# Kernel optimization log

Hardware: AMD Instinct MI355X
Metric: run time of the kernel (lower is better)

## Reference

```python
import jax, jax.numpy as jnp
import numpy as np

B, T, D_IN, H, NL = 4096, 512, 32, 16, 2


def setup_inputs() -> dict:
    key = jax.random.key(0)
    ks = jax.random.split(key, 16)
    s = lambda fan: 1.0 / np.sqrt(H)  # PyTorch LSTM init scale: U(-1/sqrt(H), 1/sqrt(H))
    u = lambda k, shape: jax.random.uniform(k, shape, jnp.float32, -s(H), s(H))
    inp = {
        "x": jax.random.normal(ks[0], (B, T, D_IN), jnp.float32),
        # layer 0 (gate order i, f, g, o as in PyTorch)
        "Wih0": u(ks[1], (4 * H, D_IN)),
        "Whh0": u(ks[2], (4 * H, H)),
        "bih0": u(ks[3], (4 * H,)),
        "bhh0": u(ks[4], (4 * H,)),
        # layer 1
        "Wih1": u(ks[5], (4 * H, H)),
        "Whh1": u(ks[6], (4 * H, H)),
        "bih1": u(ks[7], (4 * H,)),
        "bhh1": u(ks[8], (4 * H,)),
        # MLP head
        "fc1_w": u(ks[9], (8, H)),
        "fc1_b": u(ks[10], (8,)),
        "fc2_w": u(ks[11], (1, 8)),
        "fc2_b": u(ks[12], (1,)),
    }
    return inp


def _lstm_layer(x_seq, Wih, Whh, bih, bhh):
    # x_seq: [B, T, D]; returns all hidden states [B, T, H]
    b = bih + bhh
    # precompute input projections for all timesteps: [T, B, 4H]
    xg = jnp.einsum("btd,gd->tbg", x_seq, Wih) + b
    h0 = jnp.zeros((x_seq.shape[0], H), x_seq.dtype)
    c0 = jnp.zeros_like(h0)

    def step(carry, xt):
        h, c = carry
        gates = xt + h @ Whh.T  # [B, 4H]
        i, f, g, o = jnp.split(gates, 4, axis=-1)
        i, f, o = jax.nn.sigmoid(i), jax.nn.sigmoid(f), jax.nn.sigmoid(o)
        g = jnp.tanh(g)
        c = f * c + i * g
        h = o * jnp.tanh(c)
        return (h, c), h

    _, hs = jax.lax.scan(step, (h0, c0), xg)  # hs: [T, B, H]
    return jnp.transpose(hs, (1, 0, 2))


def reference(x, Wih0, Whh0, bih0, bhh0, Wih1, Whh1, bih1, bhh1, fc1_w, fc1_b, fc2_w, fc2_b):
    h1 = _lstm_layer(x, Wih0, Whh0, bih0, bhh0)   # [B, T, H]
    h2 = _lstm_layer(h1, Wih1, Whh1, bih1, bhh1)  # [B, T, H]
    last = h2[:, -1, :]                            # [B, H]
    y = jax.nn.relu(last @ fc1_w.T + fc1_b)        # [B, 8]
    return y @ fc2_w.T + fc2_b                     # [B, 1]
```

## Files before the change

kernel.cpp:

```cpp
#include <hip/hip_runtime.h>
#include <stdint.h>

#define T_STEPS 512
#define D_INP   32
#define CHUNK   8
#define NCHUNK  (T_STEPS / CHUNK)

typedef float f2 __attribute__((ext_vector_type(2)));
typedef float f4 __attribute__((ext_vector_type(4)));

typedef const uint32_t __attribute__((address_space(1)))* gas1_t;
typedef uint32_t __attribute__((address_space(3)))* las3_t;

#define LOG2E 1.44269504088896f
#define TANHK (-2.88539008177793f)

template <int K>
__device__ __forceinline__ float qbcast(float v) {
  return __int_as_float(
      __builtin_amdgcn_mov_dpp(__float_as_int(v), K * 85, 0xF, 0xF, true));
}

__device__ __forceinline__ float frcp(float v) { return __builtin_amdgcn_rcpf(v); }
__device__ __forceinline__ float fexp2(float v) { return __builtin_amdgcn_exp2f(v); }
__device__ __forceinline__ f2 lo2(f4 v) { return __builtin_shufflevector(v, v, 0, 1); }
__device__ __forceinline__ f2 hi2(f4 v) { return __builtin_shufflevector(v, v, 2, 3); }
__device__ __forceinline__ f2 pkfma(f2 a, f2 b, f2 c) {
  return __builtin_elementwise_fma(a, b, c);
}

extern "C" __global__ void __launch_bounds__(256)
lstm2_fused(const float* __restrict__ x,
            const float* __restrict__ Wih0, const float* __restrict__ Whh0,
            const float* __restrict__ bih0, const float* __restrict__ bhh0,
            const float* __restrict__ Wih1, const float* __restrict__ Whh1,
            const float* __restrict__ bih1, const float* __restrict__ bhh1,
            const float* __restrict__ fc1w, const float* __restrict__ fc1b,
            const float* __restrict__ fc2w, const float* __restrict__ fc2b,
            float* __restrict__ out)
{
  __shared__ __align__(16) float lx[4][2][CHUNK * D_INP];
  __shared__ __align__(16) float lh0[4][80];
  __shared__ __align__(16) float lh1[4][80];

  const int tid  = threadIdx.x;
  const int w    = tid >> 6;
  const int lane = tid & 63;
  const int b    = (blockIdx.x << 2) + w;

  const int k   = lane & 3;
  const int u   = lane >> 2;
  const int row = k * 16 + u;

  const float sc = (k == 2) ? -2.0f * LOG2E : -LOG2E;
  const float mA = (k == 2) ?  2.0f : 1.0f;
  const float aA = (k == 2) ? -1.0f : 0.0f;

  f2 wi0[16], wh0[8], wi1[8], wh1[8];
  {
    const f4* p = (const f4*)(Wih0 + row * 32);
#pragma unroll
    for (int q = 0; q < 8; ++q) {
      f4 v = p[q];
      wi0[2 * q + 0] = lo2(v) * sc;
      wi0[2 * q + 1] = hi2(v) * sc;
    }
    const f4* p0 = (const f4*)(Whh0 + row * 16);
    const f4* p1 = (const f4*)(Wih1 + row * 16);
    const f4* p2 = (const f4*)(Whh1 + row * 16);
#pragma unroll
    for (int q = 0; q < 4; ++q) {
      f4 a = p0[q], bq = p1[q], cq = p2[q];
      wh0[2 * q] = lo2(a) * sc;  wh0[2 * q + 1] = hi2(a) * sc;
      wi1[2 * q] = lo2(bq) * sc; wi1[2 * q + 1] = hi2(bq) * sc;
      wh1[2 * q] = lo2(cq) * sc; wh1[2 * q + 1] = hi2(cq) * sc;
    }
  }
  const float bs0 = sc * (bih0[row] + bhh0[row]);
  const float bs1 = sc * (bih1[row] + bhh1[row]);

  const int slot = (k == 0) ? u : (16 + lane);
  float* h0slot = &lh0[w][slot];
  float* h1slot = &lh1[w][slot];

  float c0 = 0.f, c1 = 0.f;
  f2 h0p[8];
#pragma unroll
  for (int j = 0; j < 8; ++j) h0p[j] = (f2){0.f, 0.f};
  if (lane < 16) lh1[w][lane] = 0.f;

  const float* xg = x + (size_t)b * (T_STEPS * D_INP);

  {
    const float* src = xg + lane * 4;
    __builtin_amdgcn_global_load_lds((gas1_t)(const void*)src,
                                     (las3_t)(void*)&lx[w][0][0], 16, 0, 0);
  }

#pragma unroll 1
  for (int c = 0; c < NCHUNK; ++c) {
    asm volatile("s_waitcnt vmcnt(0)" ::: "memory");
    if (c + 1 < NCHUNK) {
      const float* src = xg + (c + 1) * (CHUNK * D_INP) + lane * 4;
      __builtin_amdgcn_global_load_lds((gas1_t)(const void*)src,
                                       (las3_t)(void*)&lx[w][(c + 1) & 1][0],
                                       16, 0, 0);
    }
    const float* xp = &lx[w][c & 1][0];
#pragma unroll
    for (int tt = 0; tt < CHUNK; ++tt) {
      const float* xq = xp + tt * D_INP;
      f4 hA = *(const f4*)(&lh1[w][0]);
      f4 hB = *(const f4*)(&lh1[w][4]);
      f4 hC = *(const f4*)(&lh1[w][8]);
      f4 hD = *(const f4*)(&lh1[w][12]);
      f2 b01 = (f2){bs1, 0.f}, b23 = (f2){0.f, 0.f};
      b01 = pkfma(wh1[0], lo2(hA), b01);  b23 = pkfma(wh1[1], hi2(hA), b23);
      b01 = pkfma(wh1[2], lo2(hB), b01);  b23 = pkfma(wh1[3], hi2(hB), b23);
      b01 = pkfma(wh1[4], lo2(hC), b01);  b23 = pkfma(wh1[5], hi2(hC), b23);
      b01 = pkfma(wh1[6], lo2(hD), b01);  b23 = pkfma(wh1[7], hi2(hD), b23);
      f2 a01 = (f2){bs0, 0.f}, a23 = (f2){0.f, 0.f};
#pragma unroll
      for (int q = 0; q < 8; ++q) {
        f4 v = *(const f4*)(xq + 4 * q);
        a01 = pkfma(wi0[2 * q + 0], lo2(v), a01);
        a23 = pkfma(wi0[2 * q + 1], hi2(v), a23);
      }
#pragma unroll
      for (int q = 0; q < 4; ++q) {
        a01 = pkfma(wh0[2 * q + 0], h0p[2 * q + 0], a01);
        a23 = pkfma(wh0[2 * q + 1], h0p[2 * q + 1], a23);
      }
      f2 asum = a01 + a23;
      float gs = asum.x + asum.y;
      float av = fmaf(mA, frcp(1.f + fexp2(gs)), aA);
      float fv = qbcast<1>(av), gv = qbcast<2>(av), ov = qbcast<3>(av);
      c0 = fmaf(fv, c0, av * gv);
      float th = fmaf(2.f, frcp(1.f + fexp2(TANHK * c0)), -1.f);
      float h0n = ov * th;
      *h0slot = h0n;
#pragma unroll
      for (int q = 0; q < 4; ++q) {
        f4 hv = *(const f4*)(&lh0[w][4 * q]);
        h0p[2 * q + 0] = lo2(hv);
        h0p[2 * q + 1] = hi2(hv);
      }
#pragma unroll
      for (int q = 0; q < 4; ++q) {
        b01 = pkfma(wi1[2 * q + 0], h0p[2 * q + 0], b01);
        b23 = pkfma(wi1[2 * q + 1], h0p[2 * q + 1], b23);
      }
      f2 bsum = b01 + b23;
      float gs1 = bsum.x + bsum.y;
      float av1 = fmaf(mA, frcp(1.f + fexp2(gs1)), aA);
      float fv1 = qbcast<1>(av1), gv1 = qbcast<2>(av1), ov1 = qbcast<3>(av1);
      c1 = fmaf(fv1, c1, av1 * gv1);
      float th1 = fmaf(2.f, frcp(1.f + fexp2(TANHK * c1)), -1.f);
      float h1n = ov1 * th1;
      *h1slot = h1n;
    }
  }

  float h1f[16];
#pragma unroll
  for (int q = 0; q < 4; ++q) {
    f4 hv = *(const f4*)(&lh1[w][4 * q]);
#pragma unroll
    for (int r = 0; r < 4; ++r) h1f[4 * q + r] = hv[r];
  }
  float rr = 0.f;
  if (lane < 8) {
    float acc = fc1b[lane];
#pragma unroll
    for (int j = 0; j < 16; ++j) acc = fmaf(fc1w[lane * 16 + j], h1f[j], acc);
    rr = fmaxf(acc, 0.f) * fc2w[lane];
  }
  rr += __shfl_xor(rr, 1, 64);
  rr += __shfl_xor(rr, 2, 64);
  rr += __shfl_xor(rr, 4, 64);
  if (lane == 0) out[b] = rr + fc2b[0];
}

extern "C" void kernel_launch(void* const* d_in, const int* in_sizes, int n_in,
                              void* d_out, int out_size, void* d_ws, size_t ws_size,
                              hipStream_t stream) {
  (void)in_sizes; (void)n_in; (void)d_ws; (void)ws_size; (void)out_size;
  const float* x    = (const float*)d_in[0];
  const float* Wih0 = (const float*)d_in[1];
  const float* Whh0 = (const float*)d_in[2];
  const float* bih0 = (const float*)d_in[3];
  const float* bhh0 = (const float*)d_in[4];
  const float* Wih1 = (const float*)d_in[5];
  const float* Whh1 = (const float*)d_in[6];
  const float* bih1 = (const float*)d_in[7];
  const float* bhh1 = (const float*)d_in[8];
  const float* fc1w = (const float*)d_in[9];
  const float* fc1b = (const float*)d_in[10];
  const float* fc2w = (const float*)d_in[11];
  const float* fc2b = (const float*)d_in[12];
  lstm2_fused<<<dim3(1024), dim3(256), 0, stream>>>(
      x, Wih0, Whh0, bih0, bhh0, Wih1, Whh1, bih1, bhh1,
      fc1w, fc1b, fc2w, fc2b, (float*)d_out);
}
```

Baseline: 408.7 us.

## Split LSTM layers across two wavefronts with chunked LDS ring pipeline

Each block now handles one batch element with two wavefronts. Wave 0 runs layer 0 and writes each chunk of hidden states into a double-buffered LDS ring, while wave 1 runs layer 1 on the previous chunk, and the two sync once per chunk. This shortens the per-step serial dependency chain of each wave and lets the two layers overlap. The cost is twice as many waves per batch element, a block-wide barrier every chunk, and one chunk of extra pipeline latency.

```diff
diff --git a/kernel.cpp b/kernel.cpp
--- a/kernel.cpp
+++ b/kernel.cpp
@@ -29,24 +29,25 @@
   return __builtin_elementwise_fma(a, b, c);
 }
 
-extern "C" __global__ void __launch_bounds__(256)
-lstm2_fused(const float* __restrict__ x,
-            const float* __restrict__ Wih0, const float* __restrict__ Whh0,
-            const float* __restrict__ bih0, const float* __restrict__ bhh0,
-            const float* __restrict__ Wih1, const float* __restrict__ Whh1,
-            const float* __restrict__ bih1, const float* __restrict__ bhh1,
-            const float* __restrict__ fc1w, const float* __restrict__ fc1b,
-            const float* __restrict__ fc2w, const float* __restrict__ fc2b,
-            float* __restrict__ out)
+extern "C" __global__ void __launch_bounds__(128)
+lstm2_pipe(const float* __restrict__ x,
+           const float* __restrict__ Wih0, const float* __restrict__ Whh0,
+           const float* __restrict__ bih0, const float* __restrict__ bhh0,
+           const float* __restrict__ Wih1, const float* __restrict__ Whh1,
+           const float* __restrict__ bih1, const float* __restrict__ bhh1,
+           const float* __restrict__ fc1w, const float* __restrict__ fc1b,
+           const float* __restrict__ fc2w, const float* __restrict__ fc2b,
+           float* __restrict__ out)
 {
-  __shared__ __align__(16) float lx[4][2][CHUNK * D_INP];
-  __shared__ __align__(16) float lh0[4][80];
-  __shared__ __align__(16) float lh1[4][80];
+  __shared__ __align__(16) float lx[2][CHUNK * D_INP];
+  __shared__ __align__(16) float ring[2][CHUNK][16];
+  __shared__ __align__(16) float dump[64];
+  __shared__ __align__(16) float lh1[80];
 
   const int tid  = threadIdx.x;
   const int w    = tid >> 6;
   const int lane = tid & 63;
-  const int b    = (blockIdx.x << 2) + w;
+  const int b    = blockIdx.x;
 
   const int k   = lane & 3;
   const int u   = lane >> 2;
@@ -56,129 +57,165 @@
   const float mA = (k == 2) ?  2.0f : 1.0f;
   const float aA = (k == 2) ? -1.0f : 0.0f;
 
-  f2 wi0[16], wh0[8], wi1[8], wh1[8];
-  {
-    const f4* p = (const f4*)(Wih0 + row * 32);
-#pragma unroll
-    for (int q = 0; q < 8; ++q) {
-      f4 v = p[q];
-      wi0[2 * q + 0] = lo2(v) * sc;
-      wi0[2 * q + 1] = hi2(v) * sc;
-    }
-    const f4* p0 = (const f4*)(Whh0 + row * 16);
-    const f4* p1 = (const f4*)(Wih1 + row * 16);
-    const f4* p2 = (const f4*)(Whh1 + row * 16);
+  if (w == 0) {
+    f2 wi0[16], wh0[8];
+    {
+      const f4* p = (const f4*)(Wih0 + row * 32);
+#pragma unroll
+      for (int q = 0; q < 8; ++q) {
+        f4 v = p[q];
+        wi0[2 * q + 0] = lo2(v) * sc;
+        wi0[2 * q + 1] = hi2(v) * sc;
+      }
+      const f4* p0 = (const f4*)(Whh0 + row * 16);
+#pragma unroll
+      for (int q = 0; q < 4; ++q) {
+        f4 a = p0[q];
+        wh0[2 * q] = lo2(a) * sc;  wh0[2 * q + 1] = hi2(a) * sc;
+      }
+    }
+    const float bs0 = sc * (bih0[row] + bhh0[row]);
+    float c0 = 0.f;
+    if (lane < 16) ring[1][CHUNK - 1][lane] = 0.f;
+
+    const float* xg = x + (size_t)b * (T_STEPS * D_INP);
+    {
+      const float* src = xg + lane * 4;
+      __builtin_amdgcn_global_load_lds((gas1_t)(const void*)src,
+                                       (las3_t)(void*)&lx[0][0], 16, 0, 0);
+    }
+
+#pragma unroll 1
+    for (int c = 0; c <= NCHUNK; ++c) {
+      if (c < NCHUNK) {
+        asm volatile("s_waitcnt vmcnt(0)" ::: "memory");
+        if (c + 1 < NCHUNK) {
+          const float* src = xg + (c + 1) * (CHUNK * D_INP) + lane * 4;
+          __builtin_amdgcn_global_load_lds((gas1_t)(const void*)src,
+                                           (las3_t)(void*)&lx[(c + 1) & 1][0],
+                                           16, 0, 0);
+        }
+        const float* xp = &lx[c & 1][0];
+        const int h = c & 1;
+#pragma unroll
+        for (int tt = 0; tt < CHUNK; ++tt) {
+          const float* xq = xp + tt * D_INP;
+          const float* hp = (tt == 0) ? &ring[h ^ 1][CHUNK - 1][0]
+                                      : &ring[h][tt - 1][0];
+          f2 A = (f2){bs0, 0.f}, B = (f2){0.f, 0.f};
+          f2 C = (f2){0.f, 0.f}, D = (f2){0.f, 0.f};
+#pragma unroll
+          for (int q = 0; q < 4; ++q) {
+            f4 v = *(const f4*)(xq + 4 * q);
+            A = pkfma(wi0[2 * q + 0], lo2(v), A);
+            B = pkfma(wi0[2 * q + 1], hi2(v), B);
+          }
+#pragma unroll
+          for (int q = 4; q < 8; ++q) {
+            f4 v = *(const f4*)(xq + 4 * q);
+            C = pkfma(wi0[2 * q + 0], lo2(v), C);
+            D = pkfma(wi0[2 * q + 1], hi2(v), D);
+          }
+#pragma unroll
+          for (int q = 0; q < 2; ++q) {
+            f4 hv = *(const f4*)(hp + 4 * q);
+            A = pkfma(wh0[2 * q + 0], lo2(hv), A);
+            B = pkfma(wh0[2 * q + 1], hi2(hv), B);
+          }
+#pragma unroll
+          for (int q = 2; q < 4; ++q) {
+            f4 hv = *(const f4*)(hp + 4 * q);
+            C = pkfma(wh0[2 * q + 0], lo2(hv), C);
+            D = pkfma(wh0[2 * q + 1], hi2(hv), D);
+          }
+          f2 s = (A + B) + (C + D);
+          float gs = s.x + s.y;
+          float av = fmaf(mA, frcp(1.f + fexp2(gs)), aA);
+          float fv = qbcast<1>(av), gv = qbcast<2>(av), ov = qbcast<3>(av);
+          c0 = fmaf(fv, c0, av * gv);
+          float th = fmaf(2.f, frcp(1.f + fexp2(TANHK * c0)), -1.f);
+          float h0n = ov * th;
+          float* dst = (k == 0) ? &ring[h][tt][u] : &dump[lane];
+          *dst = h0n;
+        }
+      }
+      __syncthreads();
+    }
+  } else {
+    f2 wi1[8], wh1[8];
+    {
+      const f4* p1 = (const f4*)(Wih1 + row * 16);
+      const f4* p2 = (const f4*)(Whh1 + row * 16);
+#pragma unroll
+      for (int q = 0; q < 4; ++q) {
+        f4 bq = p1[q], cq = p2[q];
+        wi1[2 * q] = lo2(bq) * sc; wi1[2 * q + 1] = hi2(bq) * sc;
+        wh1[2 * q] = lo2(cq) * sc; wh1[2 * q + 1] = hi2(cq) * sc;
+      }
+    }
+    const float bs1 = sc * (bih1[row] + bhh1[row]);
+    const int slot = (k == 0) ? u : (16 + lane);
+    float* h1slot = &lh1[slot];
+    float c1 = 0.f;
+    if (lane < 16) lh1[lane] = 0.f;
+
+#pragma unroll 1
+    for (int c = 0; c <= NCHUNK; ++c) {
+      if (c >= 1) {
+        const int h = (c - 1) & 1;
+#pragma unroll
+        for (int tt = 0; tt < CHUNK; ++tt) {
+          const float* hb = &ring[h][tt][0];
+          f4 g0 = *(const f4*)(hb + 0);
+          f4 g1 = *(const f4*)(hb + 4);
+          f4 g2 = *(const f4*)(hb + 8);
+          f4 g3 = *(const f4*)(hb + 12);
+          f4 e0 = *(const f4*)(&lh1[0]);
+          f4 e1 = *(const f4*)(&lh1[4]);
+          f4 e2 = *(const f4*)(&lh1[8]);
+          f4 e3 = *(const f4*)(&lh1[12]);
+          f2 A = (f2){bs1, 0.f}, B = (f2){0.f, 0.f};
+          f2 C = (f2){0.f, 0.f}, D = (f2){0.f, 0.f};
+          A = pkfma(wi1[0], lo2(g0), A);  B = pkfma(wi1[1], hi2(g0), B);
+          A = pkfma(wi1[2], lo2(g1), A);  B = pkfma(wi1[3], hi2(g1), B);
+          C = pkfma(wi1[4], lo2(g2), C);  D = pkfma(wi1[5], hi2(g2), D);
+          C = pkfma(wi1[6], lo2(g3), C);  D = pkfma(wi1[7], hi2(g3), D);
+          A = pkfma(wh1[0], lo2(e0), A);  B = pkfma(wh1[1], hi2(e0), B);
+          A = pkfma(wh1[2], lo2(e1), A);  B = pkfma(wh1[3], hi2(e1), B);
+          C = pkfma(wh1[4], lo2(e2), C);  D = pkfma(wh1[5], hi2(e2), D);
+          C = pkfma(wh1[6], lo2(e3), C);  D = pkfma(wh1[7], hi2(e3), D);
+          f2 s = (A + B) + (C + D);
+          float gs1 = s.x + s.y;
+          float av1 = fmaf(mA, frcp(1.f + fexp2(gs1)), aA);
+          float fv1 = qbcast<1>(av1), gv1 = qbcast<2>(av1), ov1 = qbcast<3>(av1);
+          c1 = fmaf(fv1, c1, av1 * gv1);
+          float th1 = fmaf(2.f, frcp(1.f + fexp2(TANHK * c1)), -1.f);
+          float h1n = ov1 * th1;
+          *h1slot = h1n;
+        }
+      }
+      __syncthreads();
+    }
+
+    float h1f[16];
 #pragma unroll
     for (int q = 0; q < 4; ++q) {
-      f4 a = p0[q], bq = p1[q], cq = p2[q];
-      wh0[2 * q] = lo2(a) * sc;  wh0[2 * q + 1] = hi2(a) * sc;
-      wi1[2 * q] = lo2(bq) * sc; wi1[2 * q + 1] = hi2(bq) * sc;
-      wh1[2 * q] = lo2(cq) * sc; wh1[2 * q + 1] = hi2(cq) * sc;
-    }
+      f4 hv = *(const f4*)(&lh1[4 * q]);
+#pragma unroll
+      for (int r = 0; r < 4; ++r) h1f[4 * q + r] = hv[r];
+    }
+    float rr = 0.f;
+    if (lane < 8) {
+      float acc = fc1b[lane];
+#pragma unroll
+      for (int j = 0; j < 16; ++j) acc = fmaf(fc1w[lane * 16 + j], h1f[j], acc);
+      rr = fmaxf(acc, 0.f) * fc2w[lane];
+    }
+    rr += __shfl_xor(rr, 1, 64);
+    rr += __shfl_xor(rr, 2, 64);
+    rr += __shfl_xor(rr, 4, 64);
+    if (lane == 0) out[b] = rr + fc2b[0];
   }
-  const float bs0 = sc * (bih0[row] + bhh0[row]);
-  const float bs1 = sc * (bih1[row] + bhh1[row]);
-
-  const int slot = (k == 0) ? u : (16 + lane);
-  float* h0slot = &lh0[w][slot];
-  float* h1slot = &lh1[w][slot];
-
-  float c0 = 0.f, c1 = 0.f;
-  f2 h0p[8];
-#pragma unroll
-  for (int j = 0; j < 8; ++j) h0p[j] = (f2){0.f, 0.f};
-  if (lane < 16) lh1[w][lane] = 0.f;
-
-  const float* xg = x + (size_t)b * (T_STEPS * D_INP);
-
-  {
-    const float* src = xg + lane * 4;
-    __builtin_amdgcn_global_load_lds((gas1_t)(const void*)src,
-                                     (las3_t)(void*)&lx[w][0][0], 16, 0, 0);
-  }
-
-#pragma unroll 1
-  for (int c = 0; c < NCHUNK; ++c) {
-    asm volatile("s_waitcnt vmcnt(0)" ::: "memory");
-    if (c + 1 < NCHUNK) {
-      const float* src = xg + (c + 1) * (CHUNK * D_INP) + lane * 4;
-      __builtin_amdgcn_global_load_lds((gas1_t)(const void*)src,
-                                       (las3_t)(void*)&lx[w][(c + 1) & 1][0],
-                                       16, 0, 0);
-    }
-    const float* xp = &lx[w][c & 1][0];
-#pragma unroll
-    for (int tt = 0; tt < CHUNK; ++tt) {
-      const float* xq = xp + tt * D_INP;
-      f4 hA = *(const f4*)(&lh1[w][0]);
-      f4 hB = *(const f4*)(&lh1[w][4]);
-      f4 hC = *(const f4*)(&lh1[w][8]);
-      f4 hD = *(const f4*)(&lh1[w][12]);
-      f2 b01 = (f2){bs1, 0.f}, b23 = (f2){0.f, 0.f};
-      b01 = pkfma(wh1[0], lo2(hA), b01);  b23 = pkfma(wh1[1], hi2(hA), b23);
-      b01 = pkfma(wh1[2], lo2(hB), b01);  b23 = pkfma(wh1[3], hi2(hB), b23);
-      b01 = pkfma(wh1[4], lo2(hC), b01);  b23 = pkfma(wh1[5], hi2(hC), b23);
-      b01 = pkfma(wh1[6], lo2(hD), b01);  b23 = pkfma(wh1[7], hi2(hD), b23);
-      f2 a01 = (f2){bs0, 0.f}, a23 = (f2){0.f, 0.f};
-#pragma unroll
-      for (int q = 0; q < 8; ++q) {
-        f4 v = *(const f4*)(xq + 4 * q);
-        a01 = pkfma(wi0[2 * q + 0], lo2(v), a01);
-        a23 = pkfma(wi0[2 * q + 1], hi2(v), a23);
-      }
-#pragma unroll
-      for (int q = 0; q < 4; ++q) {
-        a01 = pkfma(wh0[2 * q + 0], h0p[2 * q + 0], a01);
-        a23 = pkfma(wh0[2 * q + 1], h0p[2 * q + 1], a23);
-      }
-      f2 asum = a01 + a23;
-      float gs = asum.x + asum.y;
-      float av = fmaf(mA, frcp(1.f + fexp2(gs)), aA);
-      float fv = qbcast<1>(av), gv = qbcast<2>(av), ov = qbcast<3>(av);
-      c0 = fmaf(fv, c0, av * gv);
-      float th = fmaf(2.f, frcp(1.f + fexp2(TANHK * c0)), -1.f);
-      float h0n = ov * th;
-      *h0slot = h0n;
-#pragma unroll
-      for (int q = 0; q < 4; ++q) {
-        f4 hv = *(const f4*)(&lh0[w][4 * q]);
-        h0p[2 * q + 0] = lo2(hv);
-        h0p[2 * q + 1] = hi2(hv);
-      }
-#pragma unroll
-      for (int q = 0; q < 4; ++q) {
-        b01 = pkfma(wi1[2 * q + 0], h0p[2 * q + 0], b01);
-        b23 = pkfma(wi1[2 * q + 1], h0p[2 * q + 1], b23);
-      }
-      f2 bsum = b01 + b23;
-      float gs1 = bsum.x + bsum.y;
-      float av1 = fmaf(mA, frcp(1.f + fexp2(gs1)), aA);
-      float fv1 = qbcast<1>(av1), gv1 = qbcast<2>(av1), ov1 = qbcast<3>(av1);
-      c1 = fmaf(fv1, c1, av1 * gv1);
-      float th1 = fmaf(2.f, frcp(1.f + fexp2(TANHK * c1)), -1.f);
-      float h1n = ov1 * th1;
-      *h1slot = h1n;
-    }
-  }
-
-  float h1f[16];
-#pragma unroll
-  for (int q = 0; q < 4; ++q) {
-    f4 hv = *(const f4*)(&lh1[w][4 * q]);
-#pragma unroll
-    for (int r = 0; r < 4; ++r) h1f[4 * q + r] = hv[r];
-  }
-  float rr = 0.f;
-  if (lane < 8) {
-    float acc = fc1b[lane];
-#pragma unroll
-    for (int j = 0; j < 16; ++j) acc = fmaf(fc1w[lane * 16 + j], h1f[j], acc);
-    rr = fmaxf(acc, 0.f) * fc2w[lane];
-  }
-  rr += __shfl_xor(rr, 1, 64);
-  rr += __shfl_xor(rr, 2, 64);
-  rr += __shfl_xor(rr, 4, 64);
-  if (lane == 0) out[b] = rr + fc2b[0];
 }
 
 extern "C" void kernel_launch(void* const* d_in, const int* in_sizes, int n_in,
@@ -198,7 +235,7 @@
   const float* fc1b = (const float*)d_in[10];
   const float* fc2w = (const float*)d_in[11];
   const float* fc2b = (const float*)d_in[12];
-  lstm2_fused<<<dim3(1024), dim3(256), 0, stream>>>(
+  lstm2_pipe<<<dim3(4096), dim3(128), 0, stream>>>(
       x, Wih0, Whh0, bih0, bhh0, Wih1, Whh1, bih1, bhh1,
       fc1w, fc1b, fc2w, fc2b, (float*)d_out);
 }
```

After: 492.7 us. +20.6%, slower.

## Broadcast hidden state via readlane instead of LDS, one wave per block

Applied to the files above, without the earlier changes.

Replaces the LDS round-trip for sharing h0/h1 across lanes with v_readlane broadcasts into SGPR-held scalars, and drops the LDS double-buffered async x prefetch in favour of direct per-step global loads. Launches one 64-thread block per batch element instead of four waves per block. The aim is to cut LDS write/read latency on the serial recurrence path. In exchange it adds 32 readlanes per step, gives up packed FMAs for the recurrent terms, and leaves global-load latency for x exposed with only 4x unrolling.

```diff
diff --git a/kernel.cpp b/kernel.cpp
--- a/kernel.cpp
+++ b/kernel.cpp
@@ -3,14 +3,9 @@
 
 #define T_STEPS 512
 #define D_INP   32
-#define CHUNK   8
-#define NCHUNK  (T_STEPS / CHUNK)
 
 typedef float f2 __attribute__((ext_vector_type(2)));
 typedef float f4 __attribute__((ext_vector_type(4)));
-
-typedef const uint32_t __attribute__((address_space(1)))* gas1_t;
-typedef uint32_t __attribute__((address_space(3)))* las3_t;
 
 #define LOG2E 1.44269504088896f
 #define TANHK (-2.88539008177793f)
@@ -20,7 +15,6 @@
   return __int_as_float(
       __builtin_amdgcn_mov_dpp(__float_as_int(v), K * 85, 0xF, 0xF, true));
 }
-
 __device__ __forceinline__ float frcp(float v) { return __builtin_amdgcn_rcpf(v); }
 __device__ __forceinline__ float fexp2(float v) { return __builtin_amdgcn_exp2f(v); }
 __device__ __forceinline__ f2 lo2(f4 v) { return __builtin_shufflevector(v, v, 0, 1); }
@@ -28,35 +22,32 @@
 __device__ __forceinline__ f2 pkfma(f2 a, f2 b, f2 c) {
   return __builtin_elementwise_fma(a, b, c);
 }
+__device__ __forceinline__ float rlane(float v, int l) {
+  return __int_as_float(__builtin_amdgcn_readlane(__float_as_int(v), l));
+}
 
-extern "C" __global__ void __launch_bounds__(256)
-lstm2_fused(const float* __restrict__ x,
-            const float* __restrict__ Wih0, const float* __restrict__ Whh0,
-            const float* __restrict__ bih0, const float* __restrict__ bhh0,
-            const float* __restrict__ Wih1, const float* __restrict__ Whh1,
-            const float* __restrict__ bih1, const float* __restrict__ bhh1,
-            const float* __restrict__ fc1w, const float* __restrict__ fc1b,
-            const float* __restrict__ fc2w, const float* __restrict__ fc2b,
-            float* __restrict__ out)
+extern "C" __global__ void __launch_bounds__(64)
+lstm2_rl(const float* __restrict__ x,
+         const float* __restrict__ Wih0, const float* __restrict__ Whh0,
+         const float* __restrict__ bih0, const float* __restrict__ bhh0,
+         const float* __restrict__ Wih1, const float* __restrict__ Whh1,
+         const float* __restrict__ bih1, const float* __restrict__ bhh1,
+         const float* __restrict__ fc1w, const float* __restrict__ fc1b,
+         const float* __restrict__ fc2w, const float* __restrict__ fc2b,
+         float* __restrict__ out)
 {
-  __shared__ __align__(16) float lx[4][2][CHUNK * D_INP];
-  __shared__ __align__(16) float lh0[4][80];
-  __shared__ __align__(16) float lh1[4][80];
-
-  const int tid  = threadIdx.x;
-  const int w    = tid >> 6;
-  const int lane = tid & 63;
-  const int b    = (blockIdx.x << 2) + w;
-
-  const int k   = lane & 3;
-  const int u   = lane >> 2;
-  const int row = k * 16 + u;
+  const int lane = threadIdx.x;
+  const int b    = blockIdx.x;
+  const int k    = lane & 3;
+  const int u    = lane >> 2;
+  const int row  = k * 16 + u;
 
   const float sc = (k == 2) ? -2.0f * LOG2E : -LOG2E;
   const float mA = (k == 2) ?  2.0f : 1.0f;
   const float aA = (k == 2) ? -1.0f : 0.0f;
 
-  f2 wi0[16], wh0[8], wi1[8], wh1[8];
+  f2 wi0[16];
+  float wh0[16], wi1[16], wh1[16];
   {
     const f4* p = (const f4*)(Wih0 + row * 32);
 #pragma unroll
@@ -65,114 +56,81 @@
       wi0[2 * q + 0] = lo2(v) * sc;
       wi0[2 * q + 1] = hi2(v) * sc;
     }
-    const f4* p0 = (const f4*)(Whh0 + row * 16);
-    const f4* p1 = (const f4*)(Wih1 + row * 16);
-    const f4* p2 = (const f4*)(Whh1 + row * 16);
 #pragma unroll
-    for (int q = 0; q < 4; ++q) {
-      f4 a = p0[q], bq = p1[q], cq = p2[q];
-      wh0[2 * q] = lo2(a) * sc;  wh0[2 * q + 1] = hi2(a) * sc;
-      wi1[2 * q] = lo2(bq) * sc; wi1[2 * q + 1] = hi2(bq) * sc;
-      wh1[2 * q] = lo2(cq) * sc; wh1[2 * q + 1] = hi2(cq) * sc;
+    for (int j = 0; j < 16; ++j) {
+      wh0[j] = sc * Whh0[row * 16 + j];
+      wi1[j] = sc * Wih1[row * 16 + j];
+      wh1[j] = sc * Whh1[row * 16 + j];
     }
   }
   const float bs0 = sc * (bih0[row] + bhh0[row]);
   const float bs1 = sc * (bih1[row] + bhh1[row]);
 
-  const int slot = (k == 0) ? u : (16 + lane);
-  float* h0slot = &lh0[w][slot];
-  float* h1slot = &lh1[w][slot];
+  float c0 = 0.f, c1 = 0.f;
+  float h0s[16], h1s[16];
+#pragma unroll
+  for (int j = 0; j < 16; ++j) { h0s[j] = 0.f; h1s[j] = 0.f; }
 
-  float c0 = 0.f, c1 = 0.f;
-  f2 h0p[8];
+  const float* xb = x + (size_t)b * (T_STEPS * D_INP);
+
+#pragma unroll 4
+  for (int t = 0; t < T_STEPS; ++t) {
+    const f4* xq = (const f4*)(xb + t * D_INP);
+    f2 a01 = (f2){bs0, 0.f}, a23 = (f2){0.f, 0.f};
 #pragma unroll
-  for (int j = 0; j < 8; ++j) h0p[j] = (f2){0.f, 0.f};
-  if (lane < 16) lh1[w][lane] = 0.f;
+    for (int q = 0; q < 8; ++q) {
+      f4 v = xq[q];
+      a01 = pkfma(wi0[2 * q + 0], lo2(v), a01);
+      a23 = pkfma(wi0[2 * q + 1], hi2(v), a23);
+    }
+#pragma unroll
+    for (int j = 0; j < 16; j += 4) {
+      a01.x = fmaf(wh0[j + 0], h0s[j + 0], a01.x);
+      a01.y = fmaf(wh0[j + 1], h0s[j + 1], a01.y);
+      a23.x = fmaf(wh0[j + 2], h0s[j + 2], a23.x);
+      a23.y = fmaf(wh0[j + 3], h0s[j + 3], a23.y);
+    }
+    f2 s = a01 + a23;
+    float gs = s.x + s.y;
+    float av = fmaf(mA, frcp(1.f + fexp2(gs)), aA);
+    float fv = qbcast<1>(av), gv = qbcast<2>(av), ov = qbcast<3>(av);
+    c0 = fmaf(fv, c0, av * gv);
+    float th = fmaf(2.f, frcp(1.f + fexp2(TANHK * c0)), -1.f);
+    float h0n = ov * th;
+#pragma unroll
+    for (int j = 0; j < 16; ++j) h0s[j] = rlane(h0n, 4 * j);
 
-  const float* xg = x + (size_t)b * (T_STEPS * D_INP);
-
-  {
-    const float* src = xg + lane * 4;
-    __builtin_amdgcn_global_load_lds((gas1_t)(const void*)src,
-                                     (las3_t)(void*)&lx[w][0][0], 16, 0, 0);
+    f2 b01 = (f2){bs1, 0.f}, b23 = (f2){0.f, 0.f};
+#pragma unroll
+    for (int j = 0; j < 16; j += 4) {
+      b01.x = fmaf(wi1[j + 0], h0s[j + 0], b01.x);
+      b01.y = fmaf(wi1[j + 1], h0s[j + 1], b01.y);
+      b23.x = fmaf(wi1[j + 2], h0s[j + 2], b23.x);
+      b23.y = fmaf(wi1[j + 3], h0s[j + 3], b23.y);
+    }
+#pragma unroll
+    for (int j = 0; j < 16; j += 4) {
+      b01.x = fmaf(wh1[j + 0], h1s[j + 0], b01.x);
+      b01.y = fmaf(wh1[j + 1], h1s[j + 1], b01.y);
+      b23.x = fmaf(wh1[j + 2], h1s[j + 2], b23.x);
+      b23.y = fmaf(wh1[j + 3], h1s[j + 3], b23.y);
+    }
+    f2 s1 = b01 + b23;
+    float gs1 = s1.x + s1.y;
+    float av1 = fmaf(mA, frcp(1.f + fexp2(gs1)), aA);
+    float fv1 = qbcast<1>(av1), gv1 = qbcast<2>(av1), ov1 = qbcast<3>(av1);
+    c1 = fmaf(fv1, c1, av1 * gv1);
+    float th1 = fmaf(2.f, frcp(1.f + fexp2(TANHK * c1)), -1.f);
+    float h1n = ov1 * th1;
+#pragma unroll
+    for (int j = 0; j < 16; ++j) h1s[j] = rlane(h1n, 4 * j);
   }
 
-#pragma unroll 1
-  for (int c = 0; c < NCHUNK; ++c) {
-    asm volatile("s_waitcnt vmcnt(0)" ::: "memory");
-    if (c + 1 < NCHUNK) {
-      const float* src = xg + (c + 1) * (CHUNK * D_INP) + lane * 4;
-      __builtin_amdgcn_global_load_lds((gas1_t)(const void*)src,
-                                       (las3_t)(void*)&lx[w][(c + 1) & 1][0],
-                                       16, 0, 0);
-    }
-    const float* xp = &lx[w][c & 1][0];
-#pragma unroll
-    for (int tt = 0; tt < CHUNK; ++tt) {
-      const float* xq = xp + tt * D_INP;
-      f4 hA = *(const f4*)(&lh1[w][0]);
-      f4 hB = *(const f4*)(&lh1[w][4]);
-      f4 hC = *(const f4*)(&lh1[w][8]);
-      f4 hD = *(const f4*)(&lh1[w][12]);
-      f2 b01 = (f2){bs1, 0.f}, b23 = (f2){0.f, 0.f};
-      b01 = pkfma(wh1[0], lo2(hA), b01);  b23 = pkfma(wh1[1], hi2(hA), b23);
-      b01 = pkfma(wh1[2], lo2(hB), b01);  b23 = pkfma(wh1[3], hi2(hB), b23);
-      b01 = pkfma(wh1[4], lo2(hC), b01);  b23 = pkfma(wh1[5], hi2(hC), b23);
-      b01 = pkfma(wh1[6], lo2(hD), b01);  b23 = pkfma(wh1[7], hi2(hD), b23);
-      f2 a01 = (f2){bs0, 0.f}, a23 = (f2){0.f, 0.f};
-#pragma unroll
-      for (int q = 0; q < 8; ++q) {
-        f4 v = *(const f4*)(xq + 4 * q);
-        a01 = pkfma(wi0[2 * q + 0], lo2(v), a01);
-        a23 = pkfma(wi0[2 * q + 1], hi2(v), a23);
-      }
-#pragma unroll
-      for (int q = 0; q < 4; ++q) {
-        a01 = pkfma(wh0[2 * q + 0], h0p[2 * q + 0], a01);
-        a23 = pkfma(wh0[2 * q + 1], h0p[2 * q + 1], a23);
-      }
-      f2 asum = a01 + a23;
-      float gs = asum.x + asum.y;
-      float av = fmaf(mA, frcp(1.f + fexp2(gs)), aA);
-      float fv = qbcast<1>(av), gv = qbcast<2>(av), ov = qbcast<3>(av);
-      c0 = fmaf(fv, c0, av * gv);
-      float th = fmaf(2.f, frcp(1.f + fexp2(TANHK * c0)), -1.f);
-      float h0n = ov * th;
-      *h0slot = h0n;
-#pragma unroll
-      for (int q = 0; q < 4; ++q) {
-        f4 hv = *(const f4*)(&lh0[w][4 * q]);
-        h0p[2 * q + 0] = lo2(hv);
-        h0p[2 * q + 1] = hi2(hv);
-      }
-#pragma unroll
-      for (int q = 0; q < 4; ++q) {
-        b01 = pkfma(wi1[2 * q + 0], h0p[2 * q + 0], b01);
-        b23 = pkfma(wi1[2 * q + 1], h0p[2 * q + 1], b23);
-      }
-      f2 bsum = b01 + b23;
-      float gs1 = bsum.x + bsum.y;
-      float av1 = fmaf(mA, frcp(1.f + fexp2(gs1)), aA);
-      float fv1 = qbcast<1>(av1), gv1 = qbcast<2>(av1), ov1 = qbcast<3>(av1);
-      c1 = fmaf(fv1, c1, av1 * gv1);
-      float th1 = fmaf(2.f, frcp(1.f + fexp2(TANHK * c1)), -1.f);
-      float h1n = ov1 * th1;
-      *h1slot = h1n;
-    }
-  }
-
-  float h1f[16];
-#pragma unroll
-  for (int q = 0; q < 4; ++q) {
-    f4 hv = *(const f4*)(&lh1[w][4 * q]);
-#pragma unroll
-    for (int r = 0; r < 4; ++r) h1f[4 * q + r] = hv[r];
-  }
   float rr = 0.f;
   if (lane < 8) {
     float acc = fc1b[lane];
 #pragma unroll
-    for (int j = 0; j < 16; ++j) acc = fmaf(fc1w[lane * 16 + j], h1f[j], acc);
+    for (int j = 0; j < 16; ++j) acc = fmaf(fc1w[lane * 16 + j], h1s[j], acc);
     rr = fmaxf(acc, 0.f) * fc2w[lane];
   }
   rr += __shfl_xor(rr, 1, 64);
@@ -198,7 +156,7 @@
   const float* fc1b = (const float*)d_in[10];
   const float* fc2w = (const float*)d_in[11];
   const float* fc2b = (const float*)d_in[12];
-  lstm2_fused<<<dim3(1024), dim3(256), 0, stream>>>(
+  lstm2_rl<<<dim3(4096), dim3(64), 0, stream>>>(
       x, Wih0, Whh0, bih0, bhh0, Wih1, Whh1, bih1, bhh1,
       fc1w, fc1b, fc2w, fc2b, (float*)d_out);
 }
```

After: 491.6 us. +20.3%, slower.

## Process two batch elements per wavefront to interleave independent LSTM recurrences

Applied to the files above, without the earlier changes.

Each wavefront now runs two batch elements' LSTM recurrences side by side, sharing the register-resident weights and interleaving their dependent chains for instruction-level parallelism. The grid is halved and waves_per_eu is fixed to 2, trading wave-level latency hiding for in-wave ILP. Shared-memory buffers for x chunks and hidden states are doubled per wave. This raises register pressure and relies on the compiler to actually interleave the two chains.

```diff
diff --git a/kernel.cpp b/kernel.cpp
--- a/kernel.cpp
+++ b/kernel.cpp
@@ -5,6 +5,7 @@
 #define D_INP   32
 #define CHUNK   8
 #define NCHUNK  (T_STEPS / CHUNK)
+#define ELEMS   2
 
 typedef float f2 __attribute__((ext_vector_type(2)));
 typedef float f4 __attribute__((ext_vector_type(4)));
@@ -20,7 +21,6 @@
   return __int_as_float(
       __builtin_amdgcn_mov_dpp(__float_as_int(v), K * 85, 0xF, 0xF, true));
 }
-
 __device__ __forceinline__ float frcp(float v) { return __builtin_amdgcn_rcpf(v); }
 __device__ __forceinline__ float fexp2(float v) { return __builtin_amdgcn_exp2f(v); }
 __device__ __forceinline__ f2 lo2(f4 v) { return __builtin_shufflevector(v, v, 0, 1); }
@@ -30,23 +30,24 @@
 }
 
 extern "C" __global__ void __launch_bounds__(256)
-lstm2_fused(const float* __restrict__ x,
-            const float* __restrict__ Wih0, const float* __restrict__ Whh0,
-            const float* __restrict__ bih0, const float* __restrict__ bhh0,
-            const float* __restrict__ Wih1, const float* __restrict__ Whh1,
-            const float* __restrict__ bih1, const float* __restrict__ bhh1,
-            const float* __restrict__ fc1w, const float* __restrict__ fc1b,
-            const float* __restrict__ fc2w, const float* __restrict__ fc2b,
-            float* __restrict__ out)
+__attribute__((amdgpu_waves_per_eu(2, 2)))
+lstm2_e2(const float* __restrict__ x,
+         const float* __restrict__ Wih0, const float* __restrict__ Whh0,
+         const float* __restrict__ bih0, const float* __restrict__ bhh0,
+         const float* __restrict__ Wih1, const float* __restrict__ Whh1,
+         const float* __restrict__ bih1, const float* __restrict__ bhh1,
+         const float* __restrict__ fc1w, const float* __restrict__ fc1b,
+         const float* __restrict__ fc2w, const float* __restrict__ fc2b,
+         float* __restrict__ out)
 {
-  __shared__ __align__(16) float lx[4][2][CHUNK * D_INP];
-  __shared__ __align__(16) float lh0[4][80];
-  __shared__ __align__(16) float lh1[4][80];
+  __shared__ __align__(16) float lx[4][ELEMS][2][CHUNK * D_INP];
+  __shared__ __align__(16) float lh0[4][ELEMS][80];
+  __shared__ __align__(16) float lh1[4][ELEMS][80];
 
   const int tid  = threadIdx.x;
   const int w    = tid >> 6;
   const int lane = tid & 63;
-  const int b    = (blockIdx.x << 2) + w;
+  const int base = blockIdx.x * (4 * ELEMS) + w * ELEMS;
 
   const int k   = lane & 3;
   const int u   = lane >> 2;
@@ -80,105 +81,123 @@
   const float bs1 = sc * (bih1[row] + bhh1[row]);
 
   const int slot = (k == 0) ? u : (16 + lane);
-  float* h0slot = &lh0[w][slot];
-  float* h1slot = &lh1[w][slot];
-
-  float c0 = 0.f, c1 = 0.f;
-  f2 h0p[8];
-#pragma unroll
-  for (int j = 0; j < 8; ++j) h0p[j] = (f2){0.f, 0.f};
-  if (lane < 16) lh1[w][lane] = 0.f;
-
-  const float* xg = x + (size_t)b * (T_STEPS * D_INP);
-
-  {
-    const float* src = xg + lane * 4;
+
+  float c0[ELEMS], c1[ELEMS];
+  f2 h0p[ELEMS][8];
+  float* h0slot[ELEMS];
+  float* h1slot[ELEMS];
+  const float* xg[ELEMS];
+#pragma unroll
+  for (int e = 0; e < ELEMS; ++e) {
+    c0[e] = 0.f; c1[e] = 0.f;
+#pragma unroll
+    for (int j = 0; j < 8; ++j) h0p[e][j] = (f2){0.f, 0.f};
+    h0slot[e] = &lh0[w][e][slot];
+    h1slot[e] = &lh1[w][e][slot];
+    if (lane < 16) lh1[w][e][lane] = 0.f;
+    xg[e] = x + (size_t)(base + e) * (T_STEPS * D_INP);
+    const float* src = xg[e] + lane * 4;
     __builtin_amdgcn_global_load_lds((gas1_t)(const void*)src,
-                                     (las3_t)(void*)&lx[w][0][0], 16, 0, 0);
+                                     (las3_t)(void*)&lx[w][e][0][0], 16, 0, 0);
   }
 
 #pragma unroll 1
   for (int c = 0; c < NCHUNK; ++c) {
     asm volatile("s_waitcnt vmcnt(0)" ::: "memory");
     if (c + 1 < NCHUNK) {
-      const float* src = xg + (c + 1) * (CHUNK * D_INP) + lane * 4;
-      __builtin_amdgcn_global_load_lds((gas1_t)(const void*)src,
-                                       (las3_t)(void*)&lx[w][(c + 1) & 1][0],
-                                       16, 0, 0);
-    }
-    const float* xp = &lx[w][c & 1][0];
+#pragma unroll
+      for (int e = 0; e < ELEMS; ++e) {
+        const float* src = xg[e] + (c + 1) * (CHUNK * D_INP) + lane * 4;
+        __builtin_amdgcn_global_load_lds((gas1_t)(const void*)src,
+                                         (las3_t)(void*)&lx[w][e][(c + 1) & 1][0],
+                                         16, 0, 0);
+      }
+    }
 #pragma unroll
     for (int tt = 0; tt < CHUNK; ++tt) {
-      const float* xq = xp + tt * D_INP;
-      f4 hA = *(const f4*)(&lh1[w][0]);
-      f4 hB = *(const f4*)(&lh1[w][4]);
-      f4 hC = *(const f4*)(&lh1[w][8]);
-      f4 hD = *(const f4*)(&lh1[w][12]);
-      f2 b01 = (f2){bs1, 0.f}, b23 = (f2){0.f, 0.f};
-      b01 = pkfma(wh1[0], lo2(hA), b01);  b23 = pkfma(wh1[1], hi2(hA), b23);
-      b01 = pkfma(wh1[2], lo2(hB), b01);  b23 = pkfma(wh1[3], hi2(hB), b23);
-      b01 = pkfma(wh1[4], lo2(hC), b01);  b23 = pkfma(wh1[5], hi2(hC), b23);
-      b01 = pkfma(wh1[6], lo2(hD), b01);  b23 = pkfma(wh1[7], hi2(hD), b23);
-      f2 a01 = (f2){bs0, 0.f}, a23 = (f2){0.f, 0.f};
-#pragma unroll
-      for (int q = 0; q < 8; ++q) {
-        f4 v = *(const f4*)(xq + 4 * q);
-        a01 = pkfma(wi0[2 * q + 0], lo2(v), a01);
-        a23 = pkfma(wi0[2 * q + 1], hi2(v), a23);
-      }
-#pragma unroll
-      for (int q = 0; q < 4; ++q) {
-        a01 = pkfma(wh0[2 * q + 0], h0p[2 * q + 0], a01);
-        a23 = pkfma(wh0[2 * q + 1], h0p[2 * q + 1], a23);
-      }
-      f2 asum = a01 + a23;
-      float gs = asum.x + asum.y;
-      float av = fmaf(mA, frcp(1.f + fexp2(gs)), aA);
-      float fv = qbcast<1>(av), gv = qbcast<2>(av), ov = qbcast<3>(av);
-      c0 = fmaf(fv, c0, av * gv);
-      float th = fmaf(2.f, frcp(1.f + fexp2(TANHK * c0)), -1.f);
-      float h0n = ov * th;
-      *h0slot = h0n;
-#pragma unroll
-      for (int q = 0; q < 4; ++q) {
-        f4 hv = *(const f4*)(&lh0[w][4 * q]);
-        h0p[2 * q + 0] = lo2(hv);
-        h0p[2 * q + 1] = hi2(hv);
-      }
-#pragma unroll
-      for (int q = 0; q < 4; ++q) {
-        b01 = pkfma(wi1[2 * q + 0], h0p[2 * q + 0], b01);
-        b23 = pkfma(wi1[2 * q + 1], h0p[2 * q + 1], b23);
-      }
-      f2 bsum = b01 + b23;
-      float gs1 = bsum.x + bsum.y;
-      float av1 = fmaf(mA, frcp(1.f + fexp2(gs1)), aA);
-      float fv1 = qbcast<1>(av1), gv1 = qbcast<2>(av1), ov1 = qbcast<3>(av1);
-      c1 = fmaf(fv1, c1, av1 * gv1);
-      float th1 = fmaf(2.f, frcp(1.f + fexp2(TANHK * c1)), -1.f);
-      float h1n = ov1 * th1;
-      *h1slot = h1n;
-    }
-  }
-
-  float h1f[16];
-#pragma unroll
-  for (int q = 0; q < 4; ++q) {
-    f4 hv = *(const f4*)(&lh1[w][4 * q]);
-#pragma unroll
-    for (int r = 0; r < 4; ++r) h1f[4 * q + r] = hv[r];
-  }
-  float rr = 0.f;
-  if (lane < 8) {
-    float acc = fc1b[lane];
-#pragma unroll
-    for (int j = 0; j < 16; ++j) acc = fmaf(fc1w[lane * 16 + j], h1f[j], acc);
-    rr = fmaxf(acc, 0.f) * fc2w[lane];
-  }
-  rr += __shfl_xor(rr, 1, 64);
-  rr += __shfl_xor(rr, 2, 64);
-  rr += __shfl_xor(rr, 4, 64);
-  if (lane == 0) out[b] = rr + fc2b[0];
+      f2 b01[ELEMS], b23[ELEMS];
+#pragma unroll
+      for (int e = 0; e < ELEMS; ++e) {
+        f4 hA = *(const f4*)(&lh1[w][e][0]);
+        f4 hB = *(const f4*)(&lh1[w][e][4]);
+        f4 hC = *(const f4*)(&lh1[w][e][8]);
+        f4 hD = *(const f4*)(&lh1[w][e][12]);
+        f2 p01 = (f2){bs1, 0.f}, p23 = (f2){0.f, 0.f};
+        p01 = pkfma(wh1[0], lo2(hA), p01);  p23 = pkfma(wh1[1], hi2(hA), p23);
+        p01 = pkfma(wh1[2], lo2(hB), p01);  p23 = pkfma(wh1[3], hi2(hB), p23);
+        p01 = pkfma(wh1[4], lo2(hC), p01);  p23 = pkfma(wh1[5], hi2(hC), p23);
+        p01 = pkfma(wh1[6], lo2(hD), p01);  p23 = pkfma(wh1[7], hi2(hD), p23);
+        b01[e] = p01; b23[e] = p23;
+      }
+#pragma unroll
+      for (int e = 0; e < ELEMS; ++e) {
+        const float* xq = &lx[w][e][c & 1][tt * D_INP];
+        f2 a01 = (f2){bs0, 0.f}, a23 = (f2){0.f, 0.f};
+#pragma unroll
+        for (int q = 0; q < 8; ++q) {
+          f4 v = *(const f4*)(xq + 4 * q);
+          a01 = pkfma(wi0[2 * q + 0], lo2(v), a01);
+          a23 = pkfma(wi0[2 * q + 1], hi2(v), a23);
+        }
+#pragma unroll
+        for (int q = 0; q < 4; ++q) {
+          a01 = pkfma(wh0[2 * q + 0], h0p[e][2 * q + 0], a01);
+          a23 = pkfma(wh0[2 * q + 1], h0p[e][2 * q + 1], a23);
+        }
+        f2 s = a01 + a23;
+        float gs = s.x + s.y;
+        float av = fmaf(mA, frcp(1.f + fexp2(gs)), aA);
+        float fv = qbcast<1>(av), gv = qbcast<2>(av), ov = qbcast<3>(av);
+        c0[e] = fmaf(fv, c0[e], av * gv);
+        float th = fmaf(2.f, frcp(1.f + fexp2(TANHK * c0[e])), -1.f);
+        *h0slot[e] = ov * th;
+      }
+#pragma unroll
+      for (int e = 0; e < ELEMS; ++e) {
+#pragma unroll
+        for (int q = 0; q < 4; ++q) {
+          f4 hv = *(const f4*)(&lh0[w][e][4 * q]);
+          h0p[e][2 * q + 0] = lo2(hv);
+          h0p[e][2 * q + 1] = hi2(hv);
+        }
+        f2 p01 = b01[e], p23 = b23[e];
+#pragma unroll
+        for (int q = 0; q < 4; ++q) {
+          p01 = pkfma(wi1[2 * q + 0], h0p[e][2 * q + 0], p01);
+          p23 = pkfma(wi1[2 * q + 1], h0p[e][2 * q + 1], p23);
+        }
+        f2 s1 = p01 + p23;
+        float gs1 = s1.x + s1.y;
+        float av1 = fmaf(mA, frcp(1.f + fexp2(gs1)), aA);
+        float fv1 = qbcast<1>(av1), gv1 = qbcast<2>(av1), ov1 = qbcast<3>(av1);
+        c1[e] = fmaf(fv1, c1[e], av1 * gv1);
+        float th1 = fmaf(2.f, frcp(1.f + fexp2(TANHK * c1[e])), -1.f);
+        *h1slot[e] = ov1 * th1;
+      }
+    }
+  }
+
+#pragma unroll
+  for (int e = 0; e < ELEMS; ++e) {
+    float h1f[16];
+#pragma unroll
+    for (int q = 0; q < 4; ++q) {
+      f4 hv = *(const f4*)(&lh1[w][e][4 * q]);
+#pragma unroll
+      for (int r = 0; r < 4; ++r) h1f[4 * q + r] = hv[r];
+    }
+    float rr = 0.f;
+    if (lane < 8) {
+      float acc = fc1b[lane];
+#pragma unroll
+      for (int j = 0; j < 16; ++j) acc = fmaf(fc1w[lane * 16 + j], h1f[j], acc);
+      rr = fmaxf(acc, 0.f) * fc2w[lane];
+    }
+    rr += __shfl_xor(rr, 1, 64);
+    rr += __shfl_xor(rr, 2, 64);
+    rr += __shfl_xor(rr, 4, 64);
+    if (lane == 0) out[base + e] = rr + fc2b[0];
+  }
 }
 
 extern "C" void kernel_launch(void* const* d_in, const int* in_sizes, int n_in,
@@ -198,7 +217,7 @@
   const float* fc1b = (const float*)d_in[10];
   const float* fc2w = (const float*)d_in[11];
   const float* fc2b = (const float*)d_in[12];
-  lstm2_fused<<<dim3(1024), dim3(256), 0, stream>>>(
+  lstm2_e2<<<dim3(512), dim3(256), 0, stream>>>(
       x, Wih0, Whh0, bih0, bhh0, Wih1, Whh1, bih1, bhh1,
       fc1w, fc1b, fc2w, fc2b, (float*)d_out);
 }
```

Result: slower. 459.4 us (+12.4%).
